# Optimization experiments

Hardware: AMD Instinct MI355X
Metric: run time of the kernel (lower is better)

The kernel has to match this reference:

```python
import math
import jax, jax.numpy as jnp
import numpy as np

DIM = 2048
N_HEADS = 16
HEAD_DIM = DIM // N_HEADS
HID = 5632  # multiple_of*ceil(int(2*(4*dim)/3)/multiple_of)
EPS = 1e-5
B, S = 2, 2048


def setup_inputs() -> dict:
    key = jax.random.key(0)
    ks = jax.random.split(key, 12)
    sd = 0.02
    return {
        "x": jax.random.normal(ks[0], (B, S, DIM), jnp.float32),
        "mask": jnp.zeros((1, 1, S, S), jnp.float32),
        "attn_bias": jax.random.normal(ks[1], (1, N_HEADS, S, S), jnp.float32) * 0.1,
        "wq": jax.random.normal(ks[2], (DIM, DIM), jnp.float32) * sd,
        "wk": jax.random.normal(ks[3], (DIM, DIM), jnp.float32) * sd,
        "wv": jax.random.normal(ks[4], (DIM, DIM), jnp.float32) * sd,
        "wo": jax.random.normal(ks[5], (DIM, DIM), jnp.float32) * sd,
        "w1": jax.random.normal(ks[6], (HID, DIM), jnp.float32) * sd,
        "w2": jax.random.normal(ks[7], (DIM, HID), jnp.float32) * sd,
        "w3": jax.random.normal(ks[8], (HID, DIM), jnp.float32) * sd,
        "attn_norm_w": jnp.ones((DIM,), jnp.float32),
        "ffn_norm_w": jnp.ones((DIM,), jnp.float32),
    }


def rmsnorm(x, w):
    x32 = x.astype(jnp.float32)
    y = x32 * jax.lax.rsqrt(jnp.mean(x32 * x32, axis=-1, keepdims=True) + EPS)
    return y.astype(x.dtype) * w


def reference(x, mask, attn_bias, wq, wk, wv, wo, w1, w2, w3, attn_norm_w, ffn_norm_w):
    b, s, _ = x.shape
    # --- attention ---
    h = rmsnorm(x, attn_norm_w)
    q = (h @ wq.T).reshape(b, s, N_HEADS, HEAD_DIM)
    k = (h @ wk.T).reshape(b, s, N_HEADS, HEAD_DIM)
    v = (h @ wv.T).reshape(b, s, N_HEADS, HEAD_DIM)
    scores = jnp.einsum("bqhd,bkhd->bhqk", q, k) / math.sqrt(HEAD_DIM)
    scores = scores + attn_bias + mask
    probs = jax.nn.softmax(scores.astype(jnp.float32), axis=-1).astype(q.dtype)
    out = jnp.einsum("bhqk,bkhd->bqhd", probs, v).reshape(b, s, DIM)
    h1 = x + out @ wo.T
    # --- SwiGLU FFN ---
    f = rmsnorm(h1, ffn_norm_w)
    ff = (jax.nn.silu(f @ w1.T) * (f @ w3.T)) @ w2.T
    return h1 + ff
```

## Files before the change

### kernel.cpp

```cpp
#include <hip/hip_runtime.h>
#include <stdint.h>

typedef uint16_t u16;
typedef __attribute__((ext_vector_type(8))) short s16x8;
typedef __attribute__((ext_vector_type(4))) float f32x4;

typedef const __attribute__((address_space(1))) void* gptr_t;
typedef __attribute__((address_space(3))) void* lptr_t;

__device__ __forceinline__ float bf2f(u16 u) { return __uint_as_float(((unsigned)u) << 16); }
__device__ __forceinline__ u16 f2bf(float f) {
    unsigned u = __float_as_uint(f);
    u += 0x7fffu + ((u >> 16) & 1u);
    return (u16)(u >> 16);
}
__device__ __forceinline__ void gld_lds16(const void* g, void* l) {
    __builtin_amdgcn_global_load_lds((gptr_t)g, (lptr_t)l, 16, 0, 0);
}

__global__ __launch_bounds__(256) void cvt_f32_bf16(const float* __restrict__ src,
                                                    u16* __restrict__ dst, long n)
{
    const long i = ((long)blockIdx.x * 256 + threadIdx.x) * 8;
    if (i >= n) return;
    float4 a = *(const float4*)(src + i);
    float4 b = *(const float4*)(src + i + 4);
    u16 o8[8] = { f2bf(a.x), f2bf(a.y), f2bf(a.z), f2bf(a.w),
                  f2bf(b.x), f2bf(b.y), f2bf(b.z), f2bf(b.w) };
    *(uint4*)(dst + i) = *(const uint4*)o8;
}

__global__ __launch_bounds__(256) void gemm_bt(
        const u16* __restrict__ A, const u16* __restrict__ B,
        u16* __restrict__ Cb, float* __restrict__ Cf, const float* __restrict__ Rf,
        int M, int N, int K, int ep)
{
    __shared__ __align__(16) u16 As[128 * 32];
    __shared__ __align__(16) u16 Bs[128 * 32];

    const int tid  = threadIdx.x;
    const int wave = tid >> 6, lane = tid & 63;
    const int quad = lane >> 4, l16 = lane & 15;
    const long m0 = (long)blockIdx.y * 128, n0 = (long)blockIdx.x * 128;
    const int wm = (wave >> 1) * 64, wn = (wave & 1) * 64;

    f32x4 acc[4][4] = {};

    const int c0 = tid, c1 = tid + 256;
    const u16* Ag = A + m0 * (long)K;
    const u16* Bg = B + n0 * (long)K;
    const long a0 = (long)(c0 >> 2) * K + (c0 & 3) * 8;
    const long a1 = (long)(c1 >> 2) * K + (c1 & 3) * 8;
    const int lb0 = (wave * 64) * 8;
    const int lb1 = (256 + wave * 64) * 8;

    for (int k0 = 0; k0 < K; k0 += 32) {
        __syncthreads();
        gld_lds16(Ag + a0 + k0, &As[lb0]);
        gld_lds16(Ag + a1 + k0, &As[lb1]);
        gld_lds16(Bg + a0 + k0, &Bs[lb0]);
        gld_lds16(Bg + a1 + k0, &Bs[lb1]);
        __syncthreads();

        s16x8 af[4], bfr[4];
#pragma unroll
        for (int t = 0; t < 4; t++) {
            af[t]  = *(const s16x8*)&As[(wm + t * 16 + l16) * 32 + quad * 8];
            bfr[t] = *(const s16x8*)&Bs[(wn + t * 16 + l16) * 32 + quad * 8];
        }
#pragma unroll
        for (int mt = 0; mt < 4; mt++)
#pragma unroll
            for (int nt = 0; nt < 4; nt++)
                acc[mt][nt] = __builtin_amdgcn_mfma_f32_16x16x32_bf16(
                    af[mt], bfr[nt], acc[mt][nt], 0, 0, 0);
    }

#pragma unroll
    for (int mt = 0; mt < 4; mt++)
#pragma unroll
        for (int nt = 0; nt < 4; nt++) {
            const long col = n0 + wn + nt * 16 + l16;
#pragma unroll
            for (int r = 0; r < 4; r++) {
                const long row = m0 + wm + mt * 16 + quad * 4 + r;
                const long idx = row * N + col;
                const float v = acc[mt][nt][r];
                if (ep == 0) Cb[idx] = f2bf(v);
                else         Cf[idx] = v + Rf[idx];
            }
        }
}

__global__ __launch_bounds__(256) void flash_attn(
        const u16* __restrict__ Q, const u16* __restrict__ Kp,
        const u16* __restrict__ V, const float* __restrict__ bias,
        const float* __restrict__ mask, u16* __restrict__ O)
{
    const int tid  = threadIdx.x;
    const int wave = tid >> 6, lane = tid & 63;
    const int quad = lane >> 4, l16 = lane & 15;
    const int q0 = blockIdx.x * 64, h = blockIdx.y, b = blockIdx.z;

    __shared__ __align__(16) u16 Ks[64 * 128];
    __shared__ __align__(16) u16 Vt[128 * 64];
    __shared__ __align__(16) u16 Ps[4][16 * 64];

    const long base = (long)b * 2048 * 2048 + (long)h * 128;

    s16x8 qf[4];
    {
        const u16* qp = Q + base + (long)(q0 + wave * 16 + l16) * 2048;
#pragma unroll
        for (int kk = 0; kk < 4; kk++)
            qf[kk] = *(const s16x8*)(qp + kk * 32 + quad * 8);
    }

    f32x4 oacc[8] = {};
    float m_i[4] = { -1e30f, -1e30f, -1e30f, -1e30f };
    float l_i[4] = { 0.f, 0.f, 0.f, 0.f };
    const float scale = 0.08838834764831845f;
    const int kswz = (l16 & 7) << 3;

    for (int k0 = 0; k0 < 2048; k0 += 64) {
        __syncthreads();
#pragma unroll
        for (int it = 0; it < 4; it++) {
            const int c = it * 256 + tid;
            const int row = c >> 4, col8 = (c & 15) * 8;
            const int src = col8 ^ ((row & 7) << 3);
            gld_lds16(Kp + base + (long)(k0 + row) * 2048 + src,
                      &Ks[(it * 256 + wave * 64) * 8]);
        }
#pragma unroll
        for (int it = 0; it < 4; it++) {
            const int c = it * 256 + tid;
            const int row = c >> 4, col8 = (c & 15) * 8;
            uint4 raw = *(const uint4*)(V + base + (long)(k0 + row) * 2048 + col8);
            const u16* e = (const u16*)&raw;
#pragma unroll
            for (int j = 0; j < 8; j++) {
                const int d = col8 + j;
                const int swz = ((d & 7) ^ ((d >> 3) & 7)) << 3;
                Vt[d * 64 + (row ^ swz)] = e[j];
            }
        }
        __syncthreads();

        float sv[4][4];
#pragma unroll
        for (int nt = 0; nt < 4; nt++) {
            f32x4 sa = { 0.f, 0.f, 0.f, 0.f };
#pragma unroll
            for (int kk = 0; kk < 4; kk++) {
                s16x8 kf = *(const s16x8*)&Ks[(nt * 16 + l16) * 128
                                              + ((kk * 32 + quad * 8) ^ kswz)];
                sa = __builtin_amdgcn_mfma_f32_16x16x32_bf16(qf[kk], kf, sa, 0, 0, 0);
            }
            const int kcol = k0 + nt * 16 + l16;
#pragma unroll
            for (int r = 0; r < 4; r++) {
                const int qrow = q0 + wave * 16 + quad * 4 + r;
                float val = sa[r] * scale;
                val += bias[((long)h * 2048 + qrow) * 2048 + kcol];
                val += mask[(long)qrow * 2048 + kcol];
                sv[nt][r] = val;
            }
        }

        float alpha[4];
#pragma unroll
        for (int r = 0; r < 4; r++) {
            float mx = fmaxf(fmaxf(sv[0][r], sv[1][r]), fmaxf(sv[2][r], sv[3][r]));
#pragma unroll
            for (int off = 1; off < 16; off <<= 1) mx = fmaxf(mx, __shfl_xor(mx, off));
            const float mnew = fmaxf(m_i[r], mx);
            alpha[r] = __expf(m_i[r] - mnew);
            m_i[r] = mnew;
            float rs = 0.f;
#pragma unroll
            for (int nt = 0; nt < 4; nt++) {
                const float pv = __expf(sv[nt][r] - mnew);
                sv[nt][r] = pv;
                rs += pv;
            }
#pragma unroll
            for (int off = 1; off < 16; off <<= 1) rs += __shfl_xor(rs, off);
            l_i[r] = l_i[r] * alpha[r] + rs;
        }

#pragma unroll
        for (int nt = 0; nt < 4; nt++)
#pragma unroll
            for (int r = 0; r < 4; r++) {
                const int prow = quad * 4 + r;
                Ps[wave][prow * 64 + ((nt * 16 + l16) ^ ((prow & 7) << 3))]
                    = f2bf(sv[nt][r]);
            }

#pragma unroll
        for (int dt = 0; dt < 8; dt++)
#pragma unroll
            for (int r = 0; r < 4; r++)
                oacc[dt][r] *= alpha[r];

#pragma unroll
        for (int kk2 = 0; kk2 < 2; kk2++) {
            s16x8 pf = *(const s16x8*)&Ps[wave][l16 * 64
                                               + ((kk2 * 32 + quad * 8) ^ kswz)];
#pragma unroll
            for (int dt = 0; dt < 8; dt++) {
                const int d = dt * 16 + l16;
                const int vswz = ((d & 7) ^ ((d >> 3) & 7)) << 3;
                s16x8 vf = *(const s16x8*)&Vt[d * 64
                                              + ((kk2 * 32 + quad * 8) ^ vswz)];
                oacc[dt] = __builtin_amdgcn_mfma_f32_16x16x32_bf16(pf, vf, oacc[dt], 0, 0, 0);
            }
        }
    }

#pragma unroll
    for (int dt = 0; dt < 8; dt++)
#pragma unroll
        for (int r = 0; r < 4; r++) {
            const int qrow = q0 + wave * 16 + quad * 4 + r;
            O[base + (long)qrow * 2048 + dt * 16 + l16] = f2bf(oacc[dt][r] / l_i[r]);
        }
}

__global__ __launch_bounds__(256) void rmsnorm_f32(
        const float* __restrict__ x, const float* __restrict__ w,
        u16* __restrict__ out)
{
    const int row = blockIdx.x, tid = threadIdx.x;
    const float* xr = x + (long)row * 2048;
    float4 f0 = *(const float4*)(xr + tid * 8);
    float4 f1 = *(const float4*)(xr + tid * 8 + 4);
    float v[8] = { f0.x, f0.y, f0.z, f0.w, f1.x, f1.y, f1.z, f1.w };
    float ss = 0.f;
#pragma unroll
    for (int j = 0; j < 8; j++) ss += v[j] * v[j];
#pragma unroll
    for (int off = 32; off > 0; off >>= 1) ss += __shfl_xor(ss, off);
    __shared__ float red[4];
    if ((tid & 63) == 0) red[tid >> 6] = ss;
    __syncthreads();
    const float tot = red[0] + red[1] + red[2] + red[3];
    const float sc = rsqrtf(tot * (1.0f / 2048.0f) + 1e-5f);
    float4 w0 = *(const float4*)(w + tid * 8);
    float4 w1v = *(const float4*)(w + tid * 8 + 4);
    const float wv[8] = { w0.x, w0.y, w0.z, w0.w, w1v.x, w1v.y, w1v.z, w1v.w };
    u16 o8[8];
#pragma unroll
    for (int j = 0; j < 8; j++) o8[j] = f2bf(v[j] * sc * wv[j]);
    *(uint4*)(out + (long)row * 2048 + tid * 8) = *(const uint4*)o8;
}

__global__ __launch_bounds__(256) void silu_mul(
        const u16* __restrict__ a, const u16* __restrict__ b, u16* __restrict__ g)
{
    const long i = ((long)blockIdx.x * 256 + threadIdx.x) * 8;
    uint4 ra = *(const uint4*)(a + i);
    uint4 rb = *(const uint4*)(b + i);
    const u16* ea = (const u16*)&ra;
    const u16* eb = (const u16*)&rb;
    u16 o8[8];
#pragma unroll
    for (int j = 0; j < 8; j++) {
        const float fa = bf2f(ea[j]);
        const float fb = bf2f(eb[j]);
        const float s = fa / (1.f + __expf(-fa));
        o8[j] = f2bf(s * fb);
    }
    *(uint4*)(g + i) = *(const uint4*)o8;
}

extern "C" void kernel_launch(void* const* d_in, const int* in_sizes, int n_in,
                              void* d_out, int out_size, void* d_ws, size_t ws_size,
                              hipStream_t stream)
{
    const float* x    = (const float*)d_in[0];
    const float* mask = (const float*)d_in[1];
    const float* bias = (const float*)d_in[2];
    const float* wq   = (const float*)d_in[3];
    const float* wk   = (const float*)d_in[4];
    const float* wv   = (const float*)d_in[5];
    const float* wo   = (const float*)d_in[6];
    const float* w1   = (const float*)d_in[7];
    const float* w2   = (const float*)d_in[8];
    const float* w3   = (const float*)d_in[9];
    const float* anw  = (const float*)d_in[10];
    const float* fnw  = (const float*)d_in[11];
    float* out = (float*)d_out;

    const long SZA = 2048L * 2048;
    const long SZF = 5632L * 2048;

    char* p = (char*)d_ws;
    u16* wqb = (u16*)p;  u16* wkb = wqb + SZA;  u16* wvb = wkb + SZA;
    u16* wob = wvb + SZA;
    u16* w1b = wob + SZA;  u16* w2b = w1b + SZF;  u16* w3b = w2b + SZF;
    p += (4 * SZA + 3 * SZF) * 2;
    const size_t SZ = (size_t)4096 * 2048 * 2;
    u16* h_buf = (u16*)p;  p += SZ;
    u16* q_buf = (u16*)p;  p += SZ;
    u16* k_buf = (u16*)p;  p += SZ;
    u16* v_buf = (u16*)p;  p += SZ;
    u16* s1    = (u16*)p;  p += (size_t)4096 * 5632 * 2;
    u16* s3    = (u16*)p;  p += (size_t)4096 * 5632 * 2;

    cvt_f32_bf16<<<2048, 256, 0, stream>>>(wq, wqb, SZA);
    cvt_f32_bf16<<<2048, 256, 0, stream>>>(wk, wkb, SZA);
    cvt_f32_bf16<<<2048, 256, 0, stream>>>(wv, wvb, SZA);
    cvt_f32_bf16<<<2048, 256, 0, stream>>>(wo, wob, SZA);
    cvt_f32_bf16<<<5632, 256, 0, stream>>>(w1, w1b, SZF);
    cvt_f32_bf16<<<5632, 256, 0, stream>>>(w2, w2b, SZF);
    cvt_f32_bf16<<<5632, 256, 0, stream>>>(w3, w3b, SZF);

    rmsnorm_f32<<<4096, 256, 0, stream>>>(x, anw, h_buf);
    gemm_bt<<<dim3(16, 32), 256, 0, stream>>>(h_buf, wqb, q_buf, nullptr, nullptr, 4096, 2048, 2048, 0);
    gemm_bt<<<dim3(16, 32), 256, 0, stream>>>(h_buf, wkb, k_buf, nullptr, nullptr, 4096, 2048, 2048, 0);
    gemm_bt<<<dim3(16, 32), 256, 0, stream>>>(h_buf, wvb, v_buf, nullptr, nullptr, 4096, 2048, 2048, 0);
    flash_attn<<<dim3(32, 16, 2), 256, 0, stream>>>(q_buf, k_buf, v_buf, bias, mask, h_buf);
    gemm_bt<<<dim3(16, 32), 256, 0, stream>>>(h_buf, wob, nullptr, out, x, 4096, 2048, 2048, 1);
    rmsnorm_f32<<<4096, 256, 0, stream>>>(out, fnw, q_buf);
    gemm_bt<<<dim3(44, 32), 256, 0, stream>>>(q_buf, w1b, s1, nullptr, nullptr, 4096, 5632, 2048, 0);
    gemm_bt<<<dim3(44, 32), 256, 0, stream>>>(q_buf, w3b, s3, nullptr, nullptr, 4096, 5632, 2048, 0);
    silu_mul<<<11264, 256, 0, stream>>>(s1, s3, s1);
    gemm_bt<<<dim3(16, 32), 256, 0, stream>>>(s1, w2b, nullptr, out, out, 4096, 2048, 5632, 1);
}
```

Baseline: 1.461 ms.

## Fuse QKV and W1/W3 projections into large double-buffered 256x256 GEMMs

Adds a 256x256-tile GEMM kernel with 512 threads, double-buffered LDS via global_load_lds, swizzled LDS layout, XCD-aware block remapping and setprio around the MFMA bursts. It fuses the Q/K/V projections into one N=6144 GEMM and the W1/W3 projections into one N=11264 GEMM by relying on contiguous weight buffers. Attention and the down-projection read the strided fused outputs, and silu_mul now works row-wise in place. The goal is fewer launches, more operand reuse and overlap of global loads with MFMA, at the cost of higher register and LDS pressure.

```diff
diff --git a/kernel.cpp b/kernel.cpp
--- a/kernel.cpp
+++ b/kernel.cpp
@@ -30,10 +30,106 @@
     *(uint4*)(dst + i) = *(const uint4*)o8;
 }
 
+__global__ __launch_bounds__(512, 2) void gemm256(
+        const u16* __restrict__ A, const u16* __restrict__ B,
+        u16* __restrict__ Cb, int M, int N, int K, int gx)
+{
+    __shared__ __align__(16) u16 As[2][256 * 64];
+    __shared__ __align__(16) u16 Bs[2][256 * 64];
+
+    const int tid  = threadIdx.x;
+    const int wave = tid >> 6, lane = tid & 63;
+    const int quad = lane >> 4, l16 = lane & 15;
+    const int wmi = wave >> 2, wni = wave & 3;
+
+    const int cpx = gridDim.x >> 3;
+    const int wg  = ((int)blockIdx.x & 7) * cpx + ((int)blockIdx.x >> 3);
+    const long m0 = (long)(wg / gx) * 256;
+    const long n0 = (long)(wg % gx) * 256;
+
+    f32x4 acc[8][4] = {};
+
+    const u16* Ag = A + m0 * (long)K;
+    const u16* Bg = B + n0 * (long)K;
+    long soff[4];
+    int  lbase[4];
+#pragma unroll
+    for (int i = 0; i < 4; i++) {
+        const int c = i * 512 + tid;
+        const int row = c >> 3, col8 = (c & 7) * 8;
+        soff[i]  = (long)row * K + (col8 ^ ((row & 7) << 3));
+        lbase[i] = (i * 512 + wave * 64) * 8;
+    }
+
+#pragma unroll
+    for (int i = 0; i < 4; i++) {
+        gld_lds16(Ag + soff[i], &As[0][lbase[i]]);
+        gld_lds16(Bg + soff[i], &Bs[0][lbase[i]]);
+    }
+    __syncthreads();
+
+    const int swz   = (l16 & 7) << 3;
+    const int arow0 = wmi * 128 + l16;
+    const int brow0 = wni * 64 + l16;
+
+    int db = 0;
+    for (int k0 = 0; k0 < K; k0 += 64) {
+        const int  kn = k0 + 64;
+        const bool pf = kn < K;
+        s16x8 bfrag[4][2];
+#pragma unroll
+        for (int p = 0; p < 4; p++) {
+            if (pf) {
+                gld_lds16(Ag + soff[p] + kn, &As[db ^ 1][lbase[p]]);
+                gld_lds16(Bg + soff[p] + kn, &Bs[db ^ 1][lbase[p]]);
+            }
+            if (p == 0) {
+#pragma unroll
+                for (int nt = 0; nt < 4; nt++)
+#pragma unroll
+                    for (int kk = 0; kk < 2; kk++)
+                        bfrag[nt][kk] = *(const s16x8*)&Bs[db][(brow0 + nt * 16) * 64
+                                            + ((kk * 32 + quad * 8) ^ swz)];
+            }
+            s16x8 af[2][2];
+#pragma unroll
+            for (int mtl = 0; mtl < 2; mtl++)
+#pragma unroll
+                for (int kk = 0; kk < 2; kk++)
+                    af[mtl][kk] = *(const s16x8*)&As[db][(arow0 + (2 * p + mtl) * 16) * 64
+                                        + ((kk * 32 + quad * 8) ^ swz)];
+            __builtin_amdgcn_s_setprio(1);
+#pragma unroll
+            for (int mtl = 0; mtl < 2; mtl++)
+#pragma unroll
+                for (int nt = 0; nt < 4; nt++)
+#pragma unroll
+                    for (int kk = 0; kk < 2; kk++)
+                        acc[2 * p + mtl][nt] = __builtin_amdgcn_mfma_f32_16x16x32_bf16(
+                            af[mtl][kk], bfrag[nt][kk], acc[2 * p + mtl][nt], 0, 0, 0);
+            __builtin_amdgcn_s_setprio(0);
+        }
+        __syncthreads();
+        db ^= 1;
+    }
+
+#pragma unroll
+    for (int mt = 0; mt < 8; mt++)
+#pragma unroll
+        for (int nt = 0; nt < 4; nt++) {
+            const long col = n0 + wni * 64 + nt * 16 + l16;
+#pragma unroll
+            for (int r = 0; r < 4; r++) {
+                const long row = m0 + wmi * 128 + mt * 16 + quad * 4 + r;
+                Cb[row * (long)N + col] = f2bf(acc[mt][nt][r]);
+            }
+        }
+}
+
 __global__ __launch_bounds__(256) void gemm_bt(
         const u16* __restrict__ A, const u16* __restrict__ B,
         u16* __restrict__ Cb, float* __restrict__ Cf, const float* __restrict__ Rf,
-        int M, int N, int K, int ep)
+        int M, int N, int K, int lda, int ep)
 {
     __shared__ __align__(16) u16 As[128 * 32];
     __shared__ __align__(16) u16 Bs[128 * 32];
@@ -47,19 +143,21 @@
     f32x4 acc[4][4] = {};
 
     const int c0 = tid, c1 = tid + 256;
-    const u16* Ag = A + m0 * (long)K;
+    const u16* Ag = A + m0 * (long)lda;
     const u16* Bg = B + n0 * (long)K;
-    const long a0 = (long)(c0 >> 2) * K + (c0 & 3) * 8;
-    const long a1 = (long)(c1 >> 2) * K + (c1 & 3) * 8;
+    const long aA0 = (long)(c0 >> 2) * lda + (c0 & 3) * 8;
+    const long aA1 = (long)(c1 >> 2) * lda + (c1 & 3) * 8;
+    const long aB0 = (long)(c0 >> 2) * K + (c0 & 3) * 8;
+    const long aB1 = (long)(c1 >> 2) * K + (c1 & 3) * 8;
     const int lb0 = (wave * 64) * 8;
     const int lb1 = (256 + wave * 64) * 8;
 
     for (int k0 = 0; k0 < K; k0 += 32) {
         __syncthreads();
-        gld_lds16(Ag + a0 + k0, &As[lb0]);
-        gld_lds16(Ag + a1 + k0, &As[lb1]);
-        gld_lds16(Bg + a0 + k0, &Bs[lb0]);
-        gld_lds16(Bg + a1 + k0, &Bs[lb1]);
+        gld_lds16(Ag + aA0 + k0, &As[lb0]);
+        gld_lds16(Ag + aA1 + k0, &As[lb1]);
+        gld_lds16(Bg + aB0 + k0, &Bs[lb0]);
+        gld_lds16(Bg + aB1 + k0, &Bs[lb1]);
         __syncthreads();
 
         s16x8 af[4], bfr[4];
@@ -94,7 +192,7 @@
 
 __global__ __launch_bounds__(256) void flash_attn(
         const u16* __restrict__ Q, const u16* __restrict__ Kp,
-        const u16* __restrict__ V, const float* __restrict__ bias,
+        const u16* __restrict__ V, int ld, const float* __restrict__ bias,
         const float* __restrict__ mask, u16* __restrict__ O)
 {
     const int tid  = threadIdx.x;
@@ -106,11 +204,12 @@
     __shared__ __align__(16) u16 Vt[128 * 64];
     __shared__ __align__(16) u16 Ps[4][16 * 64];
 
-    const long base = (long)b * 2048 * 2048 + (long)h * 128;
+    const long baseI = (long)b * 2048 * ld + (long)h * 128;
+    const long baseO = (long)b * 2048 * 2048 + (long)h * 128;
 
     s16x8 qf[4];
     {
-        const u16* qp = Q + base + (long)(q0 + wave * 16 + l16) * 2048;
+        const u16* qp = Q + baseI + (long)(q0 + wave * 16 + l16) * ld;
 #pragma unroll
         for (int kk = 0; kk < 4; kk++)
             qf[kk] = *(const s16x8*)(qp + kk * 32 + quad * 8);
@@ -129,20 +228,20 @@
             const int c = it * 256 + tid;
             const int row = c >> 4, col8 = (c & 15) * 8;
             const int src = col8 ^ ((row & 7) << 3);
-            gld_lds16(Kp + base + (long)(k0 + row) * 2048 + src,
+            gld_lds16(Kp + baseI + (long)(k0 + row) * ld + src,
                       &Ks[(it * 256 + wave * 64) * 8]);
         }
 #pragma unroll
         for (int it = 0; it < 4; it++) {
             const int c = it * 256 + tid;
             const int row = c >> 4, col8 = (c & 15) * 8;
-            uint4 raw = *(const uint4*)(V + base + (long)(k0 + row) * 2048 + col8);
+            uint4 raw = *(const uint4*)(V + baseI + (long)(k0 + row) * ld + col8);
             const u16* e = (const u16*)&raw;
 #pragma unroll
             for (int j = 0; j < 8; j++) {
                 const int d = col8 + j;
-                const int swz = ((d & 7) ^ ((d >> 3) & 7)) << 3;
-                Vt[d * 64 + (row ^ swz)] = e[j];
+                const int swzv = ((d & 7) ^ ((d >> 3) & 7)) << 3;
+                Vt[d * 64 + (row ^ swzv)] = e[j];
             }
         }
         __syncthreads();
@@ -224,7 +323,7 @@
 #pragma unroll
         for (int r = 0; r < 4; r++) {
             const int qrow = q0 + wave * 16 + quad * 4 + r;
-            O[base + (long)qrow * 2048 + dt * 16 + l16] = f2bf(oacc[dt][r] / l_i[r]);
+            O[baseO + (long)qrow * 2048 + dt * 16 + l16] = f2bf(oacc[dt][r] / l_i[r]);
         }
 }
 
@@ -256,14 +355,14 @@
     *(uint4*)(out + (long)row * 2048 + tid * 8) = *(const uint4*)o8;
 }
 
-__global__ __launch_bounds__(256) void silu_mul(
-        const u16* __restrict__ a, const u16* __restrict__ b, u16* __restrict__ g)
-{
-    const long i = ((long)blockIdx.x * 256 + threadIdx.x) * 8;
-    uint4 ra = *(const uint4*)(a + i);
-    uint4 rb = *(const uint4*)(b + i);
+__global__ __launch_bounds__(704) void silu_mul_rows(u16* __restrict__ s13)
+{
+    const long rb = (long)blockIdx.x * 11264;
+    const int col8 = threadIdx.x * 8;
+    uint4 ra = *(const uint4*)(s13 + rb + col8);
+    uint4 rbv = *(const uint4*)(s13 + rb + 5632 + col8);
     const u16* ea = (const u16*)&ra;
-    const u16* eb = (const u16*)&rb;
+    const u16* eb = (const u16*)&rbv;
     u16 o8[8];
 #pragma unroll
     for (int j = 0; j < 8; j++) {
@@ -272,7 +371,7 @@
         const float s = fa / (1.f + __expf(-fa));
         o8[j] = f2bf(s * fb);
     }
-    *(uint4*)(g + i) = *(const uint4*)o8;
+    *(uint4*)(s13 + rb + col8) = *(const uint4*)o8;
 }
 
 extern "C" void kernel_launch(void* const* d_in, const int* in_sizes, int n_in,
@@ -299,33 +398,30 @@
     char* p = (char*)d_ws;
     u16* wqb = (u16*)p;  u16* wkb = wqb + SZA;  u16* wvb = wkb + SZA;
     u16* wob = wvb + SZA;
-    u16* w1b = wob + SZA;  u16* w2b = w1b + SZF;  u16* w3b = w2b + SZF;
+    u16* w1b = wob + SZA;  u16* w3b = w1b + SZF;  u16* w2b = w3b + SZF;
     p += (4 * SZA + 3 * SZF) * 2;
     const size_t SZ = (size_t)4096 * 2048 * 2;
-    u16* h_buf = (u16*)p;  p += SZ;
-    u16* q_buf = (u16*)p;  p += SZ;
-    u16* k_buf = (u16*)p;  p += SZ;
-    u16* v_buf = (u16*)p;  p += SZ;
-    u16* s1    = (u16*)p;  p += (size_t)4096 * 5632 * 2;
-    u16* s3    = (u16*)p;  p += (size_t)4096 * 5632 * 2;
+    u16* h_buf  = (u16*)p;  p += SZ;
+    u16* qkv    = (u16*)p;  p += (size_t)4096 * 6144 * 2;
+    u16* s13    = (u16*)p;  p += (size_t)4096 * 11264 * 2;
 
     cvt_f32_bf16<<<2048, 256, 0, stream>>>(wq, wqb, SZA);
     cvt_f32_bf16<<<2048, 256, 0, stream>>>(wk, wkb, SZA);
     cvt_f32_bf16<<<2048, 256, 0, stream>>>(wv, wvb, SZA);
     cvt_f32_bf16<<<2048, 256, 0, stream>>>(wo, wob, SZA);
     cvt_f32_bf16<<<5632, 256, 0, stream>>>(w1, w1b, SZF);
+    cvt_f32_bf16<<<5632, 256, 0, stream>>>(w3, w3b, SZF);
     cvt_f32_bf16<<<5632, 256, 0, stream>>>(w2, w2b, SZF);
-    cvt_f32_bf16<<<5632, 256, 0, stream>>>(w3, w3b, SZF);
 
     rmsnorm_f32<<<4096, 256, 0, stream>>>(x, anw, h_buf);
-    gemm_bt<<<dim3(16, 32), 256, 0, stream>>>(h_buf, wqb, q_buf, nullptr, nullptr, 4096, 2048, 2048, 0);
-    gemm_bt<<<dim3(16, 32), 256, 0, stream>>>(h_buf, wkb, k_buf, nullptr, nullptr, 4096, 2048, 2048, 0);
-    gemm_bt<<<dim3(16, 32), 256, 0, stream>>>(h_buf, wvb, v_buf, nullptr, nullptr, 4096, 2048, 2048, 0);
-    flash_attn<<<dim3(32, 16, 2), 256, 0, stream>>>(q_buf, k_buf, v_buf, bias, mask, h_buf);
-    gemm_bt<<<dim3(16, 32), 256, 0, stream>>>(h_buf, wob, nullptr, out, x, 4096, 2048, 2048, 1);
-    rmsnorm_f32<<<4096, 256, 0, stream>>>(out, fnw, q_buf);
-    gemm_bt<<<dim3(44, 32), 256, 0, stream>>>(q_buf, w1b, s1, nullptr, nullptr, 4096, 5632, 2048, 0);
-    gemm_bt<<<dim3(44, 32), 256, 0, stream>>>(q_buf, w3b, s3, nullptr, nullptr, 4096, 5632, 2048, 0);
-    silu_mul<<<11264, 256, 0, stream>>>(s1, s3, s1);
-    gemm_bt<<<dim3(16, 32), 256, 0, stream>>>(s1, w2b, nullptr, out, out, 4096, 2048, 5632, 1);
-}
+    gemm256<<<384, 512, 0, stream>>>(h_buf, wqb, qkv, 4096, 6144, 2048, 24);
+    flash_attn<<<dim3(32, 16, 2), 256, 0, stream>>>(qkv, qkv + 2048, qkv + 4096,
+                                                    6144, bias, mask, h_buf);
+    gemm_bt<<<dim3(16, 32), 256, 0, stream>>>(h_buf, wob, nullptr, out, x,
+                                              4096, 2048, 2048, 2048, 1);
+    rmsnorm_f32<<<4096, 256, 0, stream>>>(out, fnw, h_buf);
+    gemm256<<<704, 512, 0, stream>>>(h_buf, w1b, s13, 4096, 11264, 2048, 44);
+    silu_mul_rows<<<4096, 704, 0, stream>>>(s13);
+    gemm_bt<<<dim3(16, 32), 256, 0, stream>>>(s13, w2b, nullptr, out, out,
+                                              4096, 2048, 5632, 11264, 1);
+}
```

Result: no change. 1.485 ms (+1.6%).
